# Optimization experiments

Measured on AMD Instinct MI355X. Metric: run time of the kernel, lower is better.

Reference implementation:

```python
import jax, jax.numpy as jnp
import numpy as np

B, T, D, H, DFF, E = 4, 1024, 1024, 16, 4096, 8
DH = D // H
EPS = 1e-6


def setup_inputs() -> dict:
    key = jax.random.key(0)
    ks = jax.random.split(key, 16)
    s = 0.02
    return {
        "x": jax.random.normal(ks[0], (B, T, D), jnp.float32),
        "mask": jnp.ones((B, 1, 1, T), jnp.bool_),
        "Wq": jax.random.normal(ks[1], (D, D), jnp.float32) * s,
        "bq": jnp.zeros((D,), jnp.float32),
        "Wk": jax.random.normal(ks[2], (D, D), jnp.float32) * s,
        "bk": jnp.zeros((D,), jnp.float32),
        "Wv": jax.random.normal(ks[3], (D, D), jnp.float32) * s,
        "bv": jnp.zeros((D,), jnp.float32),
        "Wo": jax.random.normal(ks[4], (D, D), jnp.float32) * s,
        "bo": jnp.zeros((D,), jnp.float32),
        "ln1_a": jnp.ones((D,), jnp.float32),
        "ln1_b": jnp.zeros((D,), jnp.float32),
        "ln2_a": jnp.ones((D,), jnp.float32),
        "ln2_b": jnp.zeros((D,), jnp.float32),
        "gW": jax.random.normal(ks[5], (D, E), jnp.float32) * s,
        "gb": jnp.zeros((E,), jnp.float32),
        "W1": jax.random.normal(ks[6], (E, D, DFF), jnp.float32) * s,
        "b1": jnp.zeros((E, DFF), jnp.float32),
        "W2": jax.random.normal(ks[7], (E, DFF, D), jnp.float32) * s,
        "b2": jnp.zeros((E, D), jnp.float32),
    }


def layer_norm(x, a, b):
    # Faithful to source: torch std is unbiased (ddof=1), divides by (std + eps)
    mean = jnp.mean(x, -1, keepdims=True)
    std = jnp.std(x, -1, keepdims=True, ddof=1)
    return a * (x - mean) / (std + EPS) + b


def mha(x, mask, Wq, bq, Wk, bk, Wv, bv, Wo, bo):
    def split(h):
        return h.reshape(B, T, H, DH).transpose(0, 2, 1, 3)  # [B,H,T,DH]
    q = split(x @ Wq + bq)
    k = split(x @ Wk + bk)
    v = split(x @ Wv + bv)
    scores = jnp.einsum("bhqd,bhkd->bhqk", q, k) / jnp.sqrt(jnp.float32(DH))
    scores = jnp.where(mask, scores, jnp.float32(-1e9))
    attn = jax.nn.softmax(scores, axis=-1)
    out = jnp.einsum("bhqk,bhkd->bhqd", attn, v)
    out = out.transpose(0, 2, 1, 3).reshape(B, T, D)
    return out @ Wo + bo


def moe(xf, gW, gb, W1, b1, W2, b2):
    # xf: [N, D] flat tokens; top-1 Switch routing
    gate_probs = jax.nn.softmax(xf @ gW + gb, axis=-1)  # [N, E]
    top1_idx = jnp.argmax(gate_probs, axis=-1)          # [N]
    top1_p = jnp.max(gate_probs, axis=-1)               # [N]
    out = jnp.zeros_like(xf)
    for e in range(E):  # fixed small structural loop over experts
        h = jax.nn.relu(xf @ W1[e] + b1[e])
        oe = h @ W2[e] + b2[e]
        sel = (top1_idx == e).astype(xf.dtype)
        out = out + (sel * top1_p)[:, None] * oe
    counts = jax.nn.one_hot(top1_idx, E, dtype=jnp.float32).sum(0)
    aux_loss = jnp.sum((counts / (B * T)) ** 2) * E
    return out, aux_loss


def reference(x, mask, Wq, bq, Wk, bk, Wv, bv, Wo, bo,
              ln1_a, ln1_b, ln2_a, ln2_b, gW, gb, W1, b1, W2, b2):
    # sublayer[0]: x + attn(norm(x))  (dropout=0, inference)
    x1 = x + mha(layer_norm(x, ln1_a, ln1_b), mask, Wq, bq, Wk, bk, Wv, bv, Wo, bo)
    # MoE applied to x1 directly (source calls feed_forward(x), not on the norm)
    ff_out, aux_loss = moe(x1.reshape(-1, D), gW, gb, W1, b1, W2, b2)
    # sublayer[1] with lambda _: ff_out  -> x1 + ff_out (norm computed but discarded)
    x2 = x1 + ff_out.reshape(B, T, D)
    return x2, aux_loss
```

## Files before the change

kernel.cpp:

```cpp
#include <hip/hip_runtime.h>

#define DEV __device__ __forceinline__

typedef unsigned short u16;
typedef __bf16 bf16x8 __attribute__((ext_vector_type(8)));
typedef float f32x4 __attribute__((ext_vector_type(4)));

static constexpr int Bn = 4, Tn = 1024, Dn = 1024, Hn = 16, DFFn = 4096, En = 8;
static constexpr int Nn = Bn * Tn;
static constexpr int MAXT = 40;
static constexpr int HROWS = 5120;

static constexpr int MT_E = 0, MT_P0 = 40, MCNT = 80, MCUR = 88, MSEG = 96, MPERM = 112;

static constexpr size_t WQKVT_O = 0;
static constexpr size_t WOT_O   = WQKVT_O + 3ull * 1024 * 1024 * 2;
static constexpr size_t W12T_O  = WOT_O + 1ull * 1024 * 1024 * 2;
static constexpr size_t X1F_O   = W12T_O + 8ull * 1024 * 4096 * 2;
static constexpr size_t XN_O    = X1F_O + (size_t)Nn * Dn * 4;
static constexpr size_t Q_O     = XN_O + (size_t)Nn * Dn * 2;
static constexpr size_t K_O     = Q_O + (size_t)Nn * Dn * 2;
static constexpr size_t VT_O    = K_O + (size_t)Nn * Dn * 2;
static constexpr size_t X1B_O   = VT_O + (size_t)Nn * Dn * 2;
static constexpr size_t P3_O    = XN_O;
static constexpr size_t H_O     = X1B_O + (size_t)Nn * Dn * 2;
static constexpr size_t TOPP_O  = H_O + (size_t)HROWS * DFFn * 2;
static constexpr size_t TIDX_O  = TOPP_O + (size_t)Nn * 4;
static constexpr size_t META_O  = TIDX_O + (size_t)Nn * 4;

DEV u16 f2bf(float f) {
  union { float f; unsigned u; } v; v.f = f;
  unsigned r = v.u + 0x7fffu + ((v.u >> 16) & 1u);
  return (u16)(r >> 16);
}

DEV void gload16(const void* g, void* l) {
  __builtin_amdgcn_global_load_lds(
      (__attribute__((address_space(1))) void*)(void*)g,
      (__attribute__((address_space(3))) void*)l, 16, 0, 0);
}

DEV void sdecode64(int o, int& row, int& c) {
  row = o >> 7;
  c = ((o >> 4) & 7) ^ (row & 7);
}

__global__ __launch_bounds__(256) void tcast_kernel(
    const float* __restrict__ src, u16* __restrict__ dst,
    int R, int C, long srcBatch, long dstBatch) {
  __shared__ u16 tile[64][65];
  src += (long)blockIdx.z * srcBatch;
  dst += (long)blockIdx.z * dstBatch;
  int r0 = blockIdx.y * 64, c0 = blockIdx.x * 64;
  int tr = threadIdx.x >> 4;
  int tc = (threadIdx.x & 15) * 4;
#pragma unroll
  for (int i = 0; i < 4; i++) {
    int r = tr + i * 16;
    float4 v = *reinterpret_cast<const float4*>(&src[(long)(r0 + r) * C + c0 + tc]);
    tile[r][tc + 0] = f2bf(v.x); tile[r][tc + 1] = f2bf(v.y);
    tile[r][tc + 2] = f2bf(v.z); tile[r][tc + 3] = f2bf(v.w);
  }
  __syncthreads();
#pragma unroll
  for (int i = 0; i < 4; i++) {
    int r = tr + i * 16;
    ushort4 o;
    o.x = tile[tc + 0][r]; o.y = tile[tc + 1][r];
    o.z = tile[tc + 2][r]; o.w = tile[tc + 3][r];
    *reinterpret_cast<ushort4*>(&dst[(long)(c0 + r) * R + r0 + tc]) = o;
  }
}

__global__ __launch_bounds__(256) void ln_kernel(
    const float* __restrict__ x, const float* __restrict__ a,
    const float* __restrict__ b, u16* __restrict__ xn) {
  __shared__ float red[8];
  int row = blockIdx.x, tid = threadIdx.x;
  int lane = tid & 63, w = tid >> 6;
  float4 v = *reinterpret_cast<const float4*>(&x[(size_t)row * 1024 + tid * 4]);
  float s = v.x + v.y + v.z + v.w;
  float sq = v.x * v.x + v.y * v.y + v.z * v.z + v.w * v.w;
#pragma unroll
  for (int sh = 1; sh <= 32; sh <<= 1) { s += __shfl_xor(s, sh); sq += __shfl_xor(sq, sh); }
  if (lane == 0) { red[w] = s; red[4 + w] = sq; }
  __syncthreads();
  s = red[0] + red[1] + red[2] + red[3];
  sq = red[4] + red[5] + red[6] + red[7];
  float mean = s * (1.0f / 1024.0f);
  float var = (sq - s * mean) * (1.0f / 1023.0f);
  float inv = 1.0f / (sqrtf(var) + 1e-6f);
  float4 av = *reinterpret_cast<const float4*>(&a[tid * 4]);
  float4 bv = *reinterpret_cast<const float4*>(&b[tid * 4]);
  ushort4 o;
  o.x = f2bf(av.x * (v.x - mean) * inv + bv.x);
  o.y = f2bf(av.y * (v.y - mean) * inv + bv.y);
  o.z = f2bf(av.z * (v.z - mean) * inv + bv.z);
  o.w = f2bf(av.w * (v.w - mean) * inv + bv.w);
  *reinterpret_cast<ushort4*>(&xn[(size_t)row * 1024 + tid * 4]) = o;
}

template <int MODE, int BM, int NG, int KSPLIT>
__global__ __launch_bounds__(256, 3) void gemm3_k(
    const u16* __restrict__ Ag, const u16* __restrict__ Bg,
    const float* __restrict__ f0, const float* __restrict__ f1,
    const float* __restrict__ f2, const float* __restrict__ xres,
    float* __restrict__ x1f, u16* __restrict__ ob0, u16* __restrict__ ob1,
    u16* __restrict__ ob2, float* __restrict__ pout, const int* __restrict__ meta) {
  constexpr int K = (MODE == 3) ? 4096 : 1024;
  constexpr int KS = K / KSPLIT;
  constexpr int NSUB = KS >> 6;
  constexpr int MT = (MODE <= 1) ? (4096 / BM) : MAXT;
  constexpr int NT = (MODE == 0) ? 24 : (MODE == 2) ? 32 : 8;
  constexpr int WR = BM / 2;
  constexpr int MI = WR / 16;
  constexpr int CA = BM / 32;

  __shared__ u16 As[BM * 64];
  __shared__ u16 Bs[128 * 64];

  const int tid = threadIdx.x, lane = tid & 63, w = tid >> 6;
  const int wm = w >> 1, wn = w & 1;
  const int cL = lane >> 4, rl15 = lane & 15;

  constexpr int NWG = MT * NT * KSPLIT;
  constexpr int q8 = NWG >> 3;
  int b = blockIdx.x;
  int lg = (b & 7) * q8 + (b >> 3);
  constexpr int PERG = KSPLIT * MT * NG;
  int g = lg / PERG, rem = lg - g * PERG;
  int s = rem / (MT * NG); rem -= s * (MT * NG);
  int mt = rem / NG;
  int nt = g * NG + (rem - (rem / NG) * NG);

  int m0 = mt * BM, n0 = nt * 128;
  const int k0 = s * KS;
  const u16* Abase = Ag;
  const u16* Bbase = Bg;
  int e = 0, cnt = 0, seg = 0, pos0 = 0;
  if (MODE >= 2) {
    e = meta[MT_E + mt];
    if (e < 0) return;
    cnt = meta[MCNT + e];
    seg = meta[MSEG + e];
    pos0 = meta[MT_P0 + mt];
    Bbase = Bg + (size_t)e * 4096 * 1024;
    if (MODE == 3) Abase = Ag + (size_t)(seg + pos0) * 4096;
    m0 = 0;
  }

  const u16* gA[CA];
  const u16* gB[4];
#pragma unroll
  for (int j = 0; j < CA; j++) {
    int row, c;
    sdecode64(j * 4096 + tid * 16, row, c);
    if constexpr (MODE == 2) {
      int pos = pos0 + row; if (pos >= cnt) pos = cnt - 1;
      int tok = meta[MPERM + seg + pos];
      gA[j] = Ag + (size_t)tok * 1024 + k0 + c * 8;
    } else {
      gA[j] = Abase + (size_t)(m0 + row) * K + k0 + c * 8;
    }
  }
#pragma unroll
  for (int j = 0; j < 4; j++) {
    int row, c;
    sdecode64(j * 4096 + tid * 16, row, c);
    gB[j] = Bbase + (size_t)(n0 + row) * K + k0 + c * 8;
  }

  auto STAGE = [&](int t) {
#pragma unroll
    for (int j = 0; j < CA; j++)
      gload16(gA[j] + t * 64, &As[j * 2048 + tid * 8]);
#pragma unroll
    for (int j = 0; j < 4; j++)
      gload16(gB[j] + t * 64, &Bs[j * 2048 + tid * 8]);
  };

  f32x4 acc[MI][4] = {};
  const char* Ab = reinterpret_cast<const char*>(&As[0]);
  const char* Bb = reinterpret_cast<const char*>(&Bs[0]);

  STAGE(0);
  for (int t = 0; t < NSUB; t++) {
    asm volatile("s_waitcnt vmcnt(0)" ::: "memory");
    __builtin_amdgcn_s_barrier();
#pragma unroll
    for (int ph = 0; ph < 2; ph++) {
      bf16x8 af[MI], bfr[4];
#pragma unroll
      for (int mi = 0; mi < MI; mi++) {
        int row = wm * WR + mi * 16 + rl15;
        af[mi] = *reinterpret_cast<const bf16x8*>(
            Ab + row * 128 + ((ph * 64 + cL * 16) ^ ((row & 7) << 4)));
      }
#pragma unroll
      for (int ni = 0; ni < 4; ni++) {
        int row = wn * 64 + ni * 16 + rl15;
        bfr[ni] = *reinterpret_cast<const bf16x8*>(
            Bb + row * 128 + ((ph * 64 + cL * 16) ^ ((row & 7) << 4)));
      }
#pragma unroll
      for (int mi = 0; mi < MI; mi++)
#pragma unroll
        for (int ni = 0; ni < 4; ni++)
          acc[mi][ni] = __builtin_amdgcn_mfma_f32_16x16x32_bf16(
              af[mi], bfr[ni], acc[mi][ni], 0, 0, 0);
    }
    __builtin_amdgcn_s_barrier();
    if (t + 1 < NSUB) STAGE(t + 1);
  }

  const int cl = rl15, rl = cL;
  if (MODE == 0) {
    int third = n0 >> 10;
    const float* bias = (third == 0) ? f0 : (third == 1) ? f1 : f2;
#pragma unroll
    for (int ni = 0; ni < 4; ni++) {
      int col = n0 + wn * 64 + ni * 16 + cl;
      int jj = col & 1023;
      float bb_ = bias[jj];
      int hh = jj >> 6, dd = jj & 63;
#pragma unroll
      for (int mi = 0; mi < MI; mi++) {
        int t0 = m0 + wm * WR + mi * 16 + rl * 4;
        int b_ = t0 >> 10, tt = t0 & 1023;
        size_t bh = (size_t)(b_ * Hn + hh);
        if (third == 2) {
          ushort4 o4;
          o4.x = f2bf(acc[mi][ni][0] + bb_); o4.y = f2bf(acc[mi][ni][1] + bb_);
          o4.z = f2bf(acc[mi][ni][2] + bb_); o4.w = f2bf(acc[mi][ni][3] + bb_);
          *reinterpret_cast<ushort4*>(&ob2[(bh * 64 + dd) * 1024 + tt]) = o4;
        } else {
          u16* dst = (third == 0) ? ob0 : ob1;
#pragma unroll
          for (int r = 0; r < 4; r++)
            dst[(bh * 1024 + tt + r) * 64 + dd] = f2bf(acc[mi][ni][r] + bb_);
        }
      }
    }
  } else if (MODE == 1) {
#pragma unroll
    for (int ni = 0; ni < 4; ni++) {
      int col = n0 + wn * 64 + ni * 16 + cl;
      float bo_ = f0[col];
#pragma unroll
      for (int mi = 0; mi < MI; mi++) {
        int row = m0 + wm * WR + mi * 16 + rl * 4;
#pragma unroll
        for (int r = 0; r < 4; r++) {
          size_t idx = (size_t)(row + r) * 1024 + col;
          float v = acc[mi][ni][r] + bo_ + xres[idx];
          x1f[idx] = v;
          ob0[idx] = f2bf(v);
        }
      }
    }
  } else if (MODE == 2) {
#pragma unroll
    for (int ni = 0; ni < 4; ni++) {
      int col = n0 + wn * 64 + ni * 16 + cl;
      float b1_ = f0[(size_t)e * 4096 + col];
#pragma unroll
      for (int mi = 0; mi < MI; mi++) {
        int pos = pos0 + wm * WR + mi * 16 + rl * 4;
#pragma unroll
        for (int r = 0; r < 4; r++) {
          float v = acc[mi][ni][r] + b1_;
          v = v > 0.0f ? v : 0.0f;
          ob0[(size_t)(seg + pos + r) * 4096 + col] = f2bf(v);
        }
      }
    }
  } else {
#pragma unroll
    for (int ni = 0; ni < 4; ni++) {
      int col = n0 + wn * 64 + ni * 16 + cl;
#pragma unroll
      for (int mi = 0; mi < MI; mi++) {
        int pos = pos0 + wm * WR + mi * 16 + rl * 4;
#pragma unroll
        for (int r = 0; r < 4; r++)
          pout[((size_t)s * HROWS + seg + pos + r) * 1024 + col] = acc[mi][ni][r];
      }
    }
  }
}

__global__ __launch_bounds__(256) void reduce3_kernel(
    const float* __restrict__ P3, const float* __restrict__ x1f,
    const float* __restrict__ topp, const float* __restrict__ b2,
    const int* __restrict__ meta, float* __restrict__ out) {
  int bidx = blockIdx.x;
  int tile = bidx >> 7, rowin = bidx & 127;
  int e = meta[MT_E + tile];
  if (e < 0) return;
  int cnt = meta[MCNT + e], seg = meta[MSEG + e];
  int pos = meta[MT_P0 + tile] + rowin;
  if (pos >= cnt) return;
  int tok = meta[MPERM + seg + pos];
  size_t prow = (size_t)(seg + pos) * 1024;
  float p = topp[tok];
  int c = threadIdx.x * 4;
  float4 a0 = *reinterpret_cast<const float4*>(&P3[prow + c]);
  float4 a1 = *reinterpret_cast<const float4*>(&P3[(size_t)HROWS * 1024 + prow + c]);
  float4 xr = *reinterpret_cast<const float4*>(&x1f[(size_t)tok * 1024 + c]);
  float4 bb = *reinterpret_cast<const float4*>(&b2[e * 1024 + c]);
  float4 o;
  o.x = xr.x + p * (a0.x + a1.x + bb.x);
  o.y = xr.y + p * (a0.y + a1.y + bb.y);
  o.z = xr.z + p * (a0.z + a1.z + bb.z);
  o.w = xr.w + p * (a0.w + a1.w + bb.w);
  *reinterpret_cast<float4*>(&out[(size_t)tok * 1024 + c]) = o;
}

__global__ __launch_bounds__(256) void attn_kernel(
    const u16* __restrict__ q, const u16* __restrict__ k,
    const u16* __restrict__ vt, u16* __restrict__ attn) {
  __shared__ u16 Ks[2][32 * 64];
  __shared__ u16 Vs[2][64 * 32];
  __shared__ u16 Ps[4][16 * 32];
  const int tid = threadIdx.x, lane = tid & 63, w = tid >> 6;
  const int bh = blockIdx.x >> 4;
  const int qt = blockIdx.x & 15;
  const size_t qkbase = (size_t)bh * Tn * 64;
  const size_t vtbase = (size_t)bh * 64 * Tn;
  const int qrow0 = qt * 64 + w * 16;

  bf16x8 qf[2];
  {
    int r = lane & 15;
    const u16* qp = q + qkbase + (size_t)(qrow0 + r) * 64 + (lane >> 4) * 8;
    qf[0] = *reinterpret_cast<const bf16x8*>(qp);
    qf[1] = *reinterpret_cast<const bf16x8*>(qp + 32);
  }
  f32x4 o[4] = {};
  float m[4] = {-1e30f, -1e30f, -1e30f, -1e30f};
  float sl[4] = {};

#define STAGE_KV(bufi, ki)                                                        \
  {                                                                               \
    int row = w * 8 + (lane >> 3);                                                \
    int sb = (lane & 7) << 4;                                                     \
    int kofs = (sb ^ ((row & 7) << 4)) >> 1;                                      \
    gload16(k + qkbase + (size_t)((ki) * 32 + row) * 64 + kofs,                   \
            &Ks[bufi][(w * 8) * 64]);                                             \
    int d = w * 16 + (lane >> 2);                                                 \
    int sb2 = (lane & 3) << 4;                                                    \
    int kofs2 = (sb2 ^ ((d & 3) << 4)) >> 1;                                      \
    gload16(vt + vtbase + (size_t)d * Tn + (ki) * 32 + kofs2,                     \
            &Vs[bufi][(w * 16) * 32]);                                            \
  }

  STAGE_KV(0, 0)
  asm volatile("s_waitcnt vmcnt(0)" ::: "memory");
  __syncthreads();
  const float scale = 0.125f;

  for (int ki = 0; ki < 32; ki++) {
    int buf = ki & 1;
    if (ki + 1 < 32) STAGE_KV(buf ^ 1, ki + 1)

    f32x4 s0 = {}, s1 = {};
#pragma unroll
    for (int hh = 0; hh < 2; hh++) {
#pragma unroll
      for (int ph = 0; ph < 2; ph++) {
        int row = hh * 16 + (lane & 15);
        int kb = ((ph * 64 + ((lane >> 4) * 16)) ^ ((row & 7) << 4));
        bf16x8 kf = *reinterpret_cast<const bf16x8*>(
            reinterpret_cast<const char*>(&Ks[buf][0]) + row * 128 + kb);
        if (hh == 0) s0 = __builtin_amdgcn_mfma_f32_16x16x32_bf16(qf[ph], kf, s0, 0, 0, 0);
        else         s1 = __builtin_amdgcn_mfma_f32_16x16x32_bf16(qf[ph], kf, s1, 0, 0, 0);
      }
    }

    float p0[4], p1[4], rsc[4];
#pragma unroll
    for (int r = 0; r < 4; r++) {
      float v0 = s0[r] * scale, v1 = s1[r] * scale;
      float mx = fmaxf(v0, v1);
#pragma unroll
      for (int sh = 1; sh <= 8; sh <<= 1) mx = fmaxf(mx, __shfl_xor(mx, sh));
      float mn = fmaxf(m[r], mx);
      rsc[r] = __expf(m[r] - mn);
      p0[r] = __expf(v0 - mn);
      p1[r] = __expf(v1 - mn);
      float rs = p0[r] + p1[r];
#pragma unroll
      for (int sh = 1; sh <= 8; sh <<= 1) rs += __shfl_xor(rs, sh);
      sl[r] = sl[r] * rsc[r] + rs;
      m[r] = mn;
    }
#pragma unroll
    for (int nf = 0; nf < 4; nf++)
#pragma unroll
      for (int r = 0; r < 4; r++) o[nf][r] *= rsc[r];

#pragma unroll
    for (int r = 0; r < 4; r++) {
      int row = (lane >> 4) * 4 + r;
      char* pb = reinterpret_cast<char*>(&Ps[w][0]) + row * 64;
      *reinterpret_cast<u16*>(pb + ((((lane & 15)) * 2) ^ ((row & 3) << 4))) = f2bf(p0[r]);
      *reinterpret_cast<u16*>(pb + (((16 + (lane & 15)) * 2) ^ ((row & 3) << 4))) = f2bf(p1[r]);
    }
    bf16x8 pf;
    {
      int row = lane & 15;
      int kb = (((lane >> 4) * 16) ^ ((row & 3) << 4));
      pf = *reinterpret_cast<const bf16x8*>(
          reinterpret_cast<const char*>(&Ps[w][0]) + row * 64 + kb);
    }
#pragma unroll
    for (int nf = 0; nf < 4; nf++) {
      int d = nf * 16 + (lane & 15);
      int kb = (((lane >> 4) * 16) ^ ((d & 3) << 4));
      bf16x8 vf = *reinterpret_cast<const bf16x8*>(
          reinterpret_cast<const char*>(&Vs[buf][0]) + d * 64 + kb);
      o[nf] = __builtin_amdgcn_mfma_f32_16x16x32_bf16(pf, vf, o[nf], 0, 0, 0);
    }
    asm volatile("s_waitcnt vmcnt(0)" ::: "memory");
    __syncthreads();
  }
#undef STAGE_KV

#pragma unroll
  for (int r = 0; r < 4; r++) {
    float inv = 1.0f / sl[r];
    int t = qrow0 + (lane >> 4) * 4 + r;
    int hcol = (bh & 15) * 64;
#pragma unroll
    for (int nf = 0; nf < 4; nf++) {
      int col = hcol + nf * 16 + (lane & 15);
      attn[((size_t)((bh >> 4) * Tn + t)) * 1024 + col] = f2bf(o[nf][r] * inv);
    }
  }
}

__global__ __launch_bounds__(256) void gate_kernel(
    const float* __restrict__ x1f, const float* __restrict__ gW,
    const float* __restrict__ gb, float* __restrict__ topp,
    int* __restrict__ tidx, int* __restrict__ meta) {
  int lane = threadIdx.x & 63;
  int n = blockIdx.x * 4 + (threadIdx.x >> 6);
  float acc[8] = {};
  const float* xr = x1f + (size_t)n * 1024;
  for (int kk = 0; kk < 16; kk++) {
    int kcol = kk * 64 + lane;
    float xv = xr[kcol];
    float4 g0 = *reinterpret_cast<const float4*>(&gW[kcol * 8]);
    float4 g1 = *reinterpret_cast<const float4*>(&gW[kcol * 8 + 4]);
    acc[0] = fmaf(xv, g0.x, acc[0]); acc[1] = fmaf(xv, g0.y, acc[1]);
    acc[2] = fmaf(xv, g0.z, acc[2]); acc[3] = fmaf(xv, g0.w, acc[3]);
    acc[4] = fmaf(xv, g1.x, acc[4]); acc[5] = fmaf(xv, g1.y, acc[5]);
    acc[6] = fmaf(xv, g1.z, acc[6]); acc[7] = fmaf(xv, g1.w, acc[7]);
  }
#pragma unroll
  for (int e2 = 0; e2 < 8; e2++)
#pragma unroll
    for (int sh = 1; sh <= 32; sh <<= 1) acc[e2] += __shfl_xor(acc[e2], sh);
  if (lane == 0) {
    float best = -1e30f; int bi = 0;
#pragma unroll
    for (int e2 = 0; e2 < 8; e2++) {
      float lg = acc[e2] + gb[e2];
      if (lg > best) { best = lg; bi = e2; }
    }
    float den = 0.0f;
#pragma unroll
    for (int e2 = 0; e2 < 8; e2++) den += __expf(acc[e2] + gb[e2] - best);
    topp[n] = 1.0f / den;
    tidx[n] = bi;
    atomicAdd(&meta[MCNT + bi], 1);
  }
}

__global__ void scan_kernel(int* meta, float* aux_out) {
  if (threadIdx.x == 0) {
    int sb = 0, t = 0;
    float aux = 0.0f;
    for (int e2 = 0; e2 < 8; e2++) {
      meta[MSEG + e2] = sb;
      int c = meta[MCNT + e2];
      int ntile = (c + 127) >> 7;
      for (int i = 0; i < ntile; i++) { meta[MT_E + t] = e2; meta[MT_P0 + t] = i * 128; t++; }
      sb += ntile << 7;
      float fr = (float)c * (1.0f / 4096.0f);
      aux += fr * fr;
    }
    for (; t < MAXT; t++) { meta[MT_E + t] = -1; meta[MT_P0 + t] = 0; }
    aux_out[0] = aux * 8.0f;
  }
}

__global__ __launch_bounds__(256) void scatter_kernel(const int* __restrict__ tidx, int* meta) {
  int n = blockIdx.x * 256 + threadIdx.x;
  int e2 = tidx[n];
  int pos = atomicAdd(&meta[MCUR + e2], 1);
  meta[MPERM + meta[MSEG + e2] + pos] = n;
}

extern "C" void kernel_launch(void* const* d_in, const int* in_sizes, int n_in,
                              void* d_out, int out_size, void* d_ws, size_t ws_size,
                              hipStream_t stream) {
  const float* x   = (const float*)d_in[0];
  const float* Wq  = (const float*)d_in[2];
  const float* bq  = (const float*)d_in[3];
  const float* Wk  = (const float*)d_in[4];
  const float* bk  = (const float*)d_in[5];
  const float* Wv  = (const float*)d_in[6];
  const float* bv  = (const float*)d_in[7];
  const float* Wo  = (const float*)d_in[8];
  const float* bo  = (const float*)d_in[9];
  const float* ln1a = (const float*)d_in[10];
  const float* ln1b = (const float*)d_in[11];
  const float* gW  = (const float*)d_in[14];
  const float* gb  = (const float*)d_in[15];
  const float* W1  = (const float*)d_in[16];
  const float* b1  = (const float*)d_in[17];
  const float* W2  = (const float*)d_in[18];
  const float* b2  = (const float*)d_in[19];
  float* out = (float*)d_out;
  char* ws = (char*)d_ws;

  u16* wqkvt = (u16*)(ws + WQKVT_O);
  u16* wot   = (u16*)(ws + WOT_O);
  u16* w12t  = (u16*)(ws + W12T_O);
  u16* xn    = (u16*)(ws + XN_O);
  u16* qb    = (u16*)(ws + Q_O);
  u16* kb    = (u16*)(ws + K_O);
  u16* vtb   = (u16*)(ws + VT_O);
  float* x1f = (float*)(ws + X1F_O);
  u16* x1b   = (u16*)(ws + X1B_O);
  float* p3  = (float*)(ws + P3_O);
  u16* hb    = (u16*)(ws + H_O);
  float* topp = (float*)(ws + TOPP_O);
  int* tidx  = (int*)(ws + TIDX_O);
  int* meta  = (int*)(ws + META_O);

  hipMemsetAsync(meta + MCNT, 0, 16 * sizeof(int), stream);

  tcast_kernel<<<dim3(16, 16, 1), 256, 0, stream>>>(Wq, wqkvt, 1024, 1024, 0, 0);
  tcast_kernel<<<dim3(16, 16, 1), 256, 0, stream>>>(Wk, wqkvt + 1024 * 1024, 1024, 1024, 0, 0);
  tcast_kernel<<<dim3(16, 16, 1), 256, 0, stream>>>(Wv, wqkvt + 2 * 1024 * 1024, 1024, 1024, 0, 0);
  tcast_kernel<<<dim3(16, 16, 1), 256, 0, stream>>>(Wo, wot, 1024, 1024, 0, 0);
  tcast_kernel<<<dim3(64, 16, 8), 256, 0, stream>>>(W1, w12t, 1024, 4096,
                                                    (long)1024 * 4096, (long)4096 * 1024);

  ln_kernel<<<4096, 256, 0, stream>>>(x, ln1a, ln1b, xn);
  gemm3_k<0, 128, 4, 1><<<768, 256, 0, stream>>>(xn, wqkvt, bq, bk, bv, nullptr, nullptr,
                                                 qb, kb, vtb, nullptr, meta);
  attn_kernel<<<1024, 256, 0, stream>>>(qb, kb, vtb, xn);
  gemm3_k<1, 64, 4, 1><<<512, 256, 0, stream>>>(xn, wot, bo, nullptr, nullptr, x, x1f,
                                                x1b, nullptr, nullptr, nullptr, meta);
  gate_kernel<<<1024, 256, 0, stream>>>(x1f, gW, gb, topp, tidx, meta);
  scan_kernel<<<1, 64, 0, stream>>>(meta, out + (size_t)Nn * Dn);
  scatter_kernel<<<16, 256, 0, stream>>>(tidx, meta);
  gemm3_k<2, 128, 4, 1><<<1280, 256, 0, stream>>>(x1b, w12t, b1, nullptr, nullptr, nullptr,
                                                  nullptr, hb, nullptr, nullptr, nullptr, meta);
  tcast_kernel<<<dim3(16, 64, 8), 256, 0, stream>>>(W2, w12t, 4096, 1024,
                                                    (long)4096 * 1024, (long)1024 * 4096);
  gemm3_k<3, 128, 2, 2><<<640, 256, 0, stream>>>(hb, w12t, b2, topp, nullptr, nullptr,
                                                 nullptr, nullptr, nullptr, nullptr, p3, meta);
  reduce3_kernel<<<MAXT * 128, 256, 0, stream>>>(p3, x1f, topp, b2, meta, out);
}
```

Baseline: 442.9 us.

## Restructure attention kernel: transposed S, register-resident P, 64-key tiles, folded Q scale

The attention kernel now computes S transposed (K as the A operand) so each lane holds probabilities for a single query, which lets P stay in registers as the B operand of the PV MFMA and removes the per-wave LDS round-trip for P. Key/value tiles grow from 32 to 64 keys with a new XOR swizzle, halving the loop trip count and the number of barriers. The 1/sqrt(dh) scale is folded into the Q projection epilogue, and block indices are remapped to group blocks across heads. Occupancy is hinted to 4 blocks per CU, which raises LDS use per block and constrains registers.

```diff
diff --git a/kernel.cpp b/kernel.cpp
--- a/kernel.cpp
+++ b/kernel.cpp
@@ -44,6 +44,8 @@
   row = o >> 7;
   c = ((o >> 4) & 7) ^ (row & 7);
 }
+
+DEV int aswz(int r, int c) { return c ^ (r & 7) ^ (((r >> 3) & 3) << 1); }
 
 __global__ __launch_bounds__(256) void tcast_kernel(
     const float* __restrict__ src, u16* __restrict__ dst,
@@ -217,6 +219,7 @@
   if (MODE == 0) {
     int third = n0 >> 10;
     const float* bias = (third == 0) ? f0 : (third == 1) ? f1 : f2;
+    const float qs = (third == 0) ? 0.125f : 1.0f;
 #pragma unroll
     for (int ni = 0; ni < 4; ni++) {
       int col = n0 + wn * 64 + ni * 16 + cl;
@@ -237,7 +240,7 @@
           u16* dst = (third == 0) ? ob0 : ob1;
 #pragma unroll
           for (int r = 0; r < 4; r++)
-            dst[(bh * 1024 + tt + r) * 64 + dd] = f2bf(acc[mi][ni][r] + bb_);
+            dst[(bh * 1024 + tt + r) * 64 + dd] = f2bf((acc[mi][ni][r] + bb_) * qs);
         }
       }
     }
@@ -316,127 +319,139 @@
   *reinterpret_cast<float4*>(&out[(size_t)tok * 1024 + c]) = o;
 }
 
-__global__ __launch_bounds__(256) void attn_kernel(
+__global__ __launch_bounds__(256, 4) void attn_kernel(
     const u16* __restrict__ q, const u16* __restrict__ k,
     const u16* __restrict__ vt, u16* __restrict__ attn) {
-  __shared__ u16 Ks[2][32 * 64];
-  __shared__ u16 Vs[2][64 * 32];
-  __shared__ u16 Ps[4][16 * 32];
+  __shared__ u16 Ks[2][64 * 64];
+  __shared__ u16 Vs[2][64 * 64];
   const int tid = threadIdx.x, lane = tid & 63, w = tid >> 6;
-  const int bh = blockIdx.x >> 4;
-  const int qt = blockIdx.x & 15;
+  const int g = lane >> 4, l15 = lane & 15;
+
+  int bb = blockIdx.x;
+  int lg = (bb & 7) * 128 + (bb >> 3);
+  const int bh = lg >> 4;
+  const int qt = lg & 15;
   const size_t qkbase = (size_t)bh * Tn * 64;
   const size_t vtbase = (size_t)bh * 64 * Tn;
   const int qrow0 = qt * 64 + w * 16;
 
   bf16x8 qf[2];
   {
-    int r = lane & 15;
-    const u16* qp = q + qkbase + (size_t)(qrow0 + r) * 64 + (lane >> 4) * 8;
+    const u16* qp = q + qkbase + (size_t)(qrow0 + l15) * 64 + g * 8;
     qf[0] = *reinterpret_cast<const bf16x8*>(qp);
     qf[1] = *reinterpret_cast<const bf16x8*>(qp + 32);
   }
+
+  const u16* gk[2];
+  const u16* gv[2];
+#pragma unroll
+  for (int j = 0; j < 2; j++) {
+    int sidx = j * 256 + tid;
+    int r = sidx >> 3, p = sidx & 7;
+    int c = aswz(r, p);
+    gk[j] = k + qkbase + (size_t)r * 64 + c * 8;
+    gv[j] = vt + vtbase + (size_t)r * Tn + c * 8;
+  }
+
+  auto STAGE = [&](int t) {
+    int buf = t & 1;
+#pragma unroll
+    for (int j = 0; j < 2; j++) {
+      int sidx = j * 256 + tid;
+      gload16(gk[j] + (size_t)t * 4096, &Ks[buf][sidx * 8]);
+      gload16(gv[j] + (size_t)t * 64, &Vs[buf][sidx * 8]);
+    }
+  };
+
   f32x4 o[4] = {};
-  float m[4] = {-1e30f, -1e30f, -1e30f, -1e30f};
-  float sl[4] = {};
-
-#define STAGE_KV(bufi, ki)                                                        \
-  {                                                                               \
-    int row = w * 8 + (lane >> 3);                                                \
-    int sb = (lane & 7) << 4;                                                     \
-    int kofs = (sb ^ ((row & 7) << 4)) >> 1;                                      \
-    gload16(k + qkbase + (size_t)((ki) * 32 + row) * 64 + kofs,                   \
-            &Ks[bufi][(w * 8) * 64]);                                             \
-    int d = w * 16 + (lane >> 2);                                                 \
-    int sb2 = (lane & 3) << 4;                                                    \
-    int kofs2 = (sb2 ^ ((d & 3) << 4)) >> 1;                                      \
-    gload16(vt + vtbase + (size_t)d * Tn + (ki) * 32 + kofs2,                     \
-            &Vs[bufi][(w * 16) * 32]);                                            \
-  }
-
-  STAGE_KV(0, 0)
-  asm volatile("s_waitcnt vmcnt(0)" ::: "memory");
-  __syncthreads();
-  const float scale = 0.125f;
-
-  for (int ki = 0; ki < 32; ki++) {
-    int buf = ki & 1;
-    if (ki + 1 < 32) STAGE_KV(buf ^ 1, ki + 1)
-
-    f32x4 s0 = {}, s1 = {};
-#pragma unroll
-    for (int hh = 0; hh < 2; hh++) {
-#pragma unroll
-      for (int ph = 0; ph < 2; ph++) {
-        int row = hh * 16 + (lane & 15);
-        int kb = ((ph * 64 + ((lane >> 4) * 16)) ^ ((row & 7) << 4));
-        bf16x8 kf = *reinterpret_cast<const bf16x8*>(
-            reinterpret_cast<const char*>(&Ks[buf][0]) + row * 128 + kb);
-        if (hh == 0) s0 = __builtin_amdgcn_mfma_f32_16x16x32_bf16(qf[ph], kf, s0, 0, 0, 0);
-        else         s1 = __builtin_amdgcn_mfma_f32_16x16x32_bf16(qf[ph], kf, s1, 0, 0, 0);
-      }
-    }
-
-    float p0[4], p1[4], rsc[4];
+  float mrun = -1e30f, lsum = 0.0f;
+
+  STAGE(0);
+  for (int t = 0; t < 16; t++) {
+    asm volatile("s_waitcnt vmcnt(0)" ::: "memory");
+    __builtin_amdgcn_s_barrier();
+    if (t + 1 < 16) STAGE(t + 1);
+
+    const char* Kb = reinterpret_cast<const char*>(&Ks[t & 1][0]);
+    const char* Vb = reinterpret_cast<const char*>(&Vs[t & 1][0]);
+
+    f32x4 sk[2][2];
+#pragma unroll
+    for (int kb = 0; kb < 2; kb++)
+#pragma unroll
+      for (int m = 0; m < 2; m++) {
+        f32x4 sa = {};
+#pragma unroll
+        for (int ph = 0; ph < 2; ph++) {
+          int ksel = kb * 32 + (l15 >> 2) * 8 + m * 4 + (lane & 3);
+          int pch = aswz(ksel, g + ph * 4);
+          bf16x8 kf = *reinterpret_cast<const bf16x8*>(Kb + ksel * 128 + pch * 16);
+          sa = __builtin_amdgcn_mfma_f32_16x16x32_bf16(kf, qf[ph], sa, 0, 0, 0);
+        }
+        sk[kb][m] = sa;
+      }
+
+    float mx = -1e30f;
+#pragma unroll
+    for (int kb = 0; kb < 2; kb++)
+#pragma unroll
+      for (int m = 0; m < 2; m++)
+#pragma unroll
+        for (int r = 0; r < 4; r++) mx = fmaxf(mx, sk[kb][m][r]);
+    mx = fmaxf(mx, __shfl_xor(mx, 16));
+    mx = fmaxf(mx, __shfl_xor(mx, 32));
+    float mn = fmaxf(mrun, mx);
+    float rsc = __expf(mrun - mn);
+    mrun = mn;
+
+    float pv[2][8];
+    float ps = 0.0f;
+#pragma unroll
+    for (int kb = 0; kb < 2; kb++)
+#pragma unroll
+      for (int m = 0; m < 2; m++)
+#pragma unroll
+        for (int r = 0; r < 4; r++) {
+          float pe = __expf(sk[kb][m][r] - mn);
+          pv[kb][m * 4 + r] = pe;
+          ps += pe;
+        }
+    ps += __shfl_xor(ps, 16);
+    ps += __shfl_xor(ps, 32);
+    lsum = lsum * rsc + ps;
+#pragma unroll
+    for (int nf = 0; nf < 4; nf++)
+#pragma unroll
+      for (int r = 0; r < 4; r++) o[nf][r] *= rsc;
+
+    bf16x8 pf[2];
+#pragma unroll
+    for (int kb = 0; kb < 2; kb++)
+#pragma unroll
+      for (int j = 0; j < 8; j++) pf[kb][j] = (__bf16)pv[kb][j];
+
+#pragma unroll
+    for (int nf = 0; nf < 4; nf++) {
+      int d = nf * 16 + l15;
+#pragma unroll
+      for (int kb = 0; kb < 2; kb++) {
+        int pch = aswz(d, g + kb * 4);
+        bf16x8 vf = *reinterpret_cast<const bf16x8*>(Vb + d * 128 + pch * 16);
+        o[nf] = __builtin_amdgcn_mfma_f32_16x16x32_bf16(vf, pf[kb], o[nf], 0, 0, 0);
+      }
+    }
+  }
+
+  float inv = 1.0f / lsum;
+  int b_ = bh >> 4, h_ = bh & 15;
+  int tok = qrow0 + l15;
+#pragma unroll
+  for (int nf = 0; nf < 4; nf++)
 #pragma unroll
     for (int r = 0; r < 4; r++) {
-      float v0 = s0[r] * scale, v1 = s1[r] * scale;
-      float mx = fmaxf(v0, v1);
-#pragma unroll
-      for (int sh = 1; sh <= 8; sh <<= 1) mx = fmaxf(mx, __shfl_xor(mx, sh));
-      float mn = fmaxf(m[r], mx);
-      rsc[r] = __expf(m[r] - mn);
-      p0[r] = __expf(v0 - mn);
-      p1[r] = __expf(v1 - mn);
-      float rs = p0[r] + p1[r];
-#pragma unroll
-      for (int sh = 1; sh <= 8; sh <<= 1) rs += __shfl_xor(rs, sh);
-      sl[r] = sl[r] * rsc[r] + rs;
-      m[r] = mn;
-    }
-#pragma unroll
-    for (int nf = 0; nf < 4; nf++)
-#pragma unroll
-      for (int r = 0; r < 4; r++) o[nf][r] *= rsc[r];
-
-#pragma unroll
-    for (int r = 0; r < 4; r++) {
-      int row = (lane >> 4) * 4 + r;
-      char* pb = reinterpret_cast<char*>(&Ps[w][0]) + row * 64;
-      *reinterpret_cast<u16*>(pb + ((((lane & 15)) * 2) ^ ((row & 3) << 4))) = f2bf(p0[r]);
-      *reinterpret_cast<u16*>(pb + (((16 + (lane & 15)) * 2) ^ ((row & 3) << 4))) = f2bf(p1[r]);
-    }
-    bf16x8 pf;
-    {
-      int row = lane & 15;
-      int kb = (((lane >> 4) * 16) ^ ((row & 3) << 4));
-      pf = *reinterpret_cast<const bf16x8*>(
-          reinterpret_cast<const char*>(&Ps[w][0]) + row * 64 + kb);
-    }
-#pragma unroll
-    for (int nf = 0; nf < 4; nf++) {
-      int d = nf * 16 + (lane & 15);
-      int kb = (((lane >> 4) * 16) ^ ((d & 3) << 4));
-      bf16x8 vf = *reinterpret_cast<const bf16x8*>(
-          reinterpret_cast<const char*>(&Vs[buf][0]) + d * 64 + kb);
-      o[nf] = __builtin_amdgcn_mfma_f32_16x16x32_bf16(pf, vf, o[nf], 0, 0, 0);
-    }
-    asm volatile("s_waitcnt vmcnt(0)" ::: "memory");
-    __syncthreads();
-  }
-#undef STAGE_KV
-
-#pragma unroll
-  for (int r = 0; r < 4; r++) {
-    float inv = 1.0f / sl[r];
-    int t = qrow0 + (lane >> 4) * 4 + r;
-    int hcol = (bh & 15) * 64;
-#pragma unroll
-    for (int nf = 0; nf < 4; nf++) {
-      int col = hcol + nf * 16 + (lane & 15);
-      attn[((size_t)((bh >> 4) * Tn + t)) * 1024 + col] = f2bf(o[nf][r] * inv);
-    }
-  }
+      int d = nf * 16 + g * 4 + r;
+      attn[((size_t)(b_ * Tn + tok)) * 1024 + h_ * 64 + d] = f2bf(o[nf][r] * inv);
+    }
 }
 
 __global__ __launch_bounds__(256) void gate_kernel(
@@ -465,8 +480,8 @@
     float best = -1e30f; int bi = 0;
 #pragma unroll
     for (int e2 = 0; e2 < 8; e2++) {
-      float lg = acc[e2] + gb[e2];
-      if (lg > best) { best = lg; bi = e2; }
+      float lgt = acc[e2] + gb[e2];
+      if (lgt > best) { best = lgt; bi = e2; }
     }
     float den = 0.0f;
 #pragma unroll
```

Result: faster. 393.3 us (-11.2%).
